# Performance work log

Measured on AMD Instinct MI355X. Metric: run time of the kernel, lower is better.

Reference implementation:

```python
import jax, jax.numpy as jnp
import numpy as np

EPS = 1e-5

def _ln(x, g, b):
    m = x.mean(-1, keepdims=True)
    v = x.var(-1, keepdims=True)
    return (x - m) / jnp.sqrt(v + EPS) * g + b

def _ln_na(x):
    m = x.mean(-1, keepdims=True)
    v = x.var(-1, keepdims=True)
    return (x - m) / jnp.sqrt(v + EPS)

def setup_inputs() -> dict:
    key = jax.random.key(0)
    ks = jax.random.split(key, 12)
    B, J, D, H, E, Z = 128, 4096, 64, 128, 256, 32
    s = 0.05
    return {
        "x": jax.random.normal(ks[0], (B, J), jnp.float32),
        "mask": jax.random.randint(ks[1], (B, J), 0, 2, jnp.int32),
        "feature_embedding": jax.random.normal(ks[2], (J, D), jnp.float32),
        "hW1": jax.random.normal(ks[3], (1 + D, H), jnp.float32) * s,
        "hb1": jnp.zeros((H,), jnp.float32),
        "hg1": jnp.ones((H,), jnp.float32),
        "hbt1": jnp.zeros((H,), jnp.float32),
        "hW2": jax.random.normal(ks[4], (H, D), jnp.float32) * s,
        "hb2": jnp.zeros((D,), jnp.float32),
        "hg2": jnp.ones((D,), jnp.float32),
        "hbt2": jnp.zeros((D,), jnp.float32),
        "eW1": jax.random.normal(ks[5], (D, E), jnp.float32) * s,
        "eb1": jnp.zeros((E,), jnp.float32),
        "eW2": jax.random.normal(ks[6], (E, 2 * Z), jnp.float32) * s,
        "eb2": jnp.zeros((2 * Z,), jnp.float32),
    }

def reference(x, mask, feature_embedding, hW1, hb1, hg1, hbt1, hW2, hb2, hg2, hbt2, eW1, eb1, eW2, eb2):
    B, J = x.shape
    D = feature_embedding.shape[1]
    m = (mask > 0).astype(x.dtype)  # (B, J)
    # per-(b,j) MLP on [x_bj, F_j]; masked entries are zeroed before pooling,
    # which equals the original gather-then-MLP-then-sum over observed entries.
    F = jnp.broadcast_to(feature_embedding[None], (B, J, D))
    h_in = jnp.concatenate([x[..., None], F], axis=-1)        # (B, J, 1+D)
    h = jax.nn.relu(_ln(h_in @ hW1 + hb1, hg1, hbt1))          # (B, J, H)
    h = jax.nn.relu(_ln(h @ hW2 + hb2, hg2, hbt2))             # (B, J, D)
    pooled = jnp.einsum('bjd,bj->bd', h, m)                    # sum over observed
    cnt = jnp.maximum(m.sum(-1, keepdims=True), 1.0)
    c = pooled / cnt                                           # mean pool; zeros if no obs
    # FCLayers (2 layers, LayerNorm w/o affine, ReLU each layer)
    e = jax.nn.relu(_ln_na(c @ eW1 + eb1))                     # (B, E)
    out = jax.nn.relu(_ln_na(e @ eW2 + eb2))                   # (B, 2Z)
    mu, logvar = jnp.split(out, 2, axis=-1)
    return (mu, logvar)
```

## Files before the change

### kernel.cpp

```cpp
#include <hip/hip_runtime.h>
#include <hip/hip_bf16.h>

#define B_  128
#define J_  4096
#define D_  64
#define H_  128
#define E_  256
#define Z_  32

typedef __attribute__((ext_vector_type(8))) short short8;
typedef __attribute__((ext_vector_type(4))) float floatx4;

#define OFF_G      0u
#define OFF_GSTATS 2097152u
#define OFF_SCAL   2162688u
#define OFF_W0C    2162944u
#define OFF_C3     2163456u
#define OFF_W2F    2163968u
#define OFF_POOL   2180352u

static __device__ __forceinline__ unsigned pk2(float a, float b) {
    __hip_bfloat162 t = __float22bfloat162_rn(make_float2(a, b));
    union { __hip_bfloat162 h; unsigned u; } c; c.h = t; return c.u;
}

__global__ __launch_bounds__(128) void g_kernel(
    const float* __restrict__ F, const float* __restrict__ hW1,
    const float* __restrict__ hb1, const float* __restrict__ hg1,
    float* __restrict__ Gp, float4* __restrict__ Gstats)
{
    const int j = blockIdx.x;
    const int h = threadIdx.x;
    const float* frow = F + (size_t)j * D_;
    float a0 = hb1[h], a1 = 0.f, a2 = 0.f, a3 = 0.f;
#pragma unroll
    for (int d = 0; d < D_; d += 4) {
        a0 = fmaf(frow[d + 0], hW1[(d + 1) * H_ + h], a0);
        a1 = fmaf(frow[d + 1], hW1[(d + 2) * H_ + h], a1);
        a2 = fmaf(frow[d + 2], hW1[(d + 3) * H_ + h], a2);
        a3 = fmaf(frow[d + 3], hW1[(d + 4) * H_ + h], a3);
    }
    const float acc = (a0 + a1) + (a2 + a3);

    const float w0h = hW1[h];
    float s1 = acc, s2 = w0h * acc, s3 = acc * acc;
#pragma unroll
    for (int off = 32; off; off >>= 1) {
        s1 += __shfl_xor(s1, off);
        s2 += __shfl_xor(s2, off);
        s3 += __shfl_xor(s3, off);
    }
    __shared__ float red[6];
    if ((h & 63) == 0) {
        int w = h >> 6;
        red[w*3+0] = s1; red[w*3+1] = s2; red[w*3+2] = s3;
    }
    __syncthreads();
    const float inv = 1.f / (float)H_;
    const float mG = (red[0] + red[3]) * inv;
    if (h == 0)
        Gstats[j] = make_float4(mG, (red[1]+red[4])*inv, (red[2]+red[5])*inv, 0.f);
    Gp[j * H_ + h] = (acc - mG) * hg1[h];
}

__global__ __launch_bounds__(256) void prep_kernel(
    const float* __restrict__ hW1, const float* __restrict__ hg1,
    const float* __restrict__ hbt1, const float* __restrict__ hW2,
    float* __restrict__ scal, float* __restrict__ w0c, float* __restrict__ c3,
    uint4* __restrict__ w2f, float4* __restrict__ pooled4)
{
    const int t = threadIdx.x;
    if (blockIdx.x > 0) {
        pooled4[(blockIdx.x - 1) * 256 + t] = make_float4(0.f, 0.f, 0.f, 0.f);
        return;
    }

    __shared__ float sred[4];
    if (t < H_) {
        const float w0h = hW1[t];
        float s = w0h, q = w0h * w0h;
#pragma unroll
        for (int off = 32; off; off >>= 1) {
            s += __shfl_xor(s, off);
            q += __shfl_xor(q, off);
        }
        if ((t & 63) == 0) { sred[(t >> 6) * 2] = s; sred[(t >> 6) * 2 + 1] = q; }
    }
    __syncthreads();
    const float mw0  = (sred[0] + sred[2]) * (1.f / (float)H_);
    const float ew02 = (sred[1] + sred[3]) * (1.f / (float)H_);
    if (t == 0) { scal[0] = mw0; scal[1] = ew02; }
    if (t < H_) {
        w0c[t] = (hW1[t] - mw0) * hg1[t];
        c3[t]  = hbt1[t];
    }

    const int lane = t & 63, wq = t >> 6;
    const int quad = lane >> 4, col = lane & 15;
    for (int f = wq; f < 16; f += 4) {
        const int kstep = f >> 2, nt = f & 3;
        const int kbase = kstep * 32 + quad * 8;
        const int n = nt * 16 + col;
        unsigned r[4];
#pragma unroll
        for (int p = 0; p < 4; p++)
            r[p] = pk2(hW2[(kbase + 2*p) * D_ + n], hW2[(kbase + 2*p + 1) * D_ + n]);
        w2f[f * 64 + lane] = make_uint4(r[0], r[1], r[2], r[3]);
    }
}

#define TPW 2
#define BB  4

__global__ __launch_bounds__(256, 2) void main_kernel(
    const float* __restrict__ x, const int* __restrict__ mask,
    const float* __restrict__ Gp, const float4* __restrict__ Gstats,
    const float* __restrict__ scal,
    const float* __restrict__ w0c, const float* __restrict__ c3,
    const uint4* __restrict__ w2f,
    const float* __restrict__ hb2, const float* __restrict__ hg2,
    const float* __restrict__ hbt2,
    float* __restrict__ pooled)
{
    const int tid  = threadIdx.x;
    const int lane = tid & 63;
    const int wv   = tid >> 6;
    const int quad = lane >> 4;
    const int col  = lane & 15;
    const int b0   = blockIdx.y * BB;

    short8 w2r[16];
#pragma unroll
    for (int f = 0; f < 16; f++) {
        union { uint4 v; short8 s; } c; c.v = w2f[f * 64 + lane];
        w2r[f] = c.s;
    }
    float4 wc[4][2], cc[4][2];
#pragma unroll
    for (int k = 0; k < 4; k++) {
        wc[k][0] = ((const float4*)(w0c + k*32 + quad*8))[0];
        wc[k][1] = ((const float4*)(w0c + k*32 + quad*8))[1];
        cc[k][0] = ((const float4*)(c3  + k*32 + quad*8))[0];
        cc[k][1] = ((const float4*)(c3  + k*32 + quad*8))[1];
    }
    float hb2v[4], g2v[4], bt2v[4];
#pragma unroll
    for (int nt = 0; nt < 4; nt++) {
        hb2v[nt] = hb2[nt*16 + col];
        g2v[nt]  = hg2[nt*16 + col];
        bt2v[nt] = hbt2[nt*16 + col];
    }
    const float mw0s  = scal[0];
    const float ew02s = scal[1];

    float pool[BB][4];
#pragma unroll
    for (int bb = 0; bb < BB; bb++)
#pragma unroll
        for (int nt = 0; nt < 4; nt++) pool[bb][nt] = 0.f;

    for (int t = 0; t < TPW; t++) {
        const int tIdx = (blockIdx.x * 4 + wv) * TPW + t;
        const int j0   = tIdx * 16;
        const int rowA = j0 + col;

        const float4 gs = Gstats[rowA];
        float xv[BB]; int4 mk[BB];
#pragma unroll
        for (int bb = 0; bb < BB; bb++) {
            xv[bb] = x[(size_t)(b0 + bb) * J_ + rowA];
            mk[bb] = *(const int4*)(mask + (size_t)(b0 + bb) * J_ + j0 + quad * 4);
        }
        const float* gpr = Gp + rowA * H_ + quad * 8;
        float4 ga[4][2];
#pragma unroll
        for (int k = 0; k < 4; k++) {
            ga[k][0] = ((const float4*)(gpr + k*32))[0];
            ga[k][1] = ((const float4*)(gpr + k*32))[1];
        }

#pragma unroll
        for (int bb = 0; bb < BB; bb++) {
            const float xA = xv[bb];
            const float mean = fmaf(xA, mw0s, gs.x);
            const float eh2  = fmaf(xA, fmaf(xA, ew02s, 2.f * gs.y), gs.z);
            const float r1   = rsqrtf(fmaf(-mean, mean, eh2) + 1e-5f);

            floatx4 acc[4];
#pragma unroll
            for (int nt = 0; nt < 4; nt++) acc[nt] = (floatx4){0.f, 0.f, 0.f, 0.f};

#pragma unroll
            for (int k = 0; k < 4; k++) {
                const float h0 = fmaxf(0.f, fmaf(fmaf(xA, wc[k][0].x, ga[k][0].x), r1, cc[k][0].x));
                const float h1 = fmaxf(0.f, fmaf(fmaf(xA, wc[k][0].y, ga[k][0].y), r1, cc[k][0].y));
                const float h2 = fmaxf(0.f, fmaf(fmaf(xA, wc[k][0].z, ga[k][0].z), r1, cc[k][0].z));
                const float h3 = fmaxf(0.f, fmaf(fmaf(xA, wc[k][0].w, ga[k][0].w), r1, cc[k][0].w));
                const float h4 = fmaxf(0.f, fmaf(fmaf(xA, wc[k][1].x, ga[k][1].x), r1, cc[k][1].x));
                const float h5 = fmaxf(0.f, fmaf(fmaf(xA, wc[k][1].y, ga[k][1].y), r1, cc[k][1].y));
                const float h6 = fmaxf(0.f, fmaf(fmaf(xA, wc[k][1].z, ga[k][1].z), r1, cc[k][1].z));
                const float h7 = fmaxf(0.f, fmaf(fmaf(xA, wc[k][1].w, ga[k][1].w), r1, cc[k][1].w));
                union { unsigned u[4]; short8 s; } af;
                af.u[0] = pk2(h0, h1);
                af.u[1] = pk2(h2, h3);
                af.u[2] = pk2(h4, h5);
                af.u[3] = pk2(h6, h7);
                acc[0] = __builtin_amdgcn_mfma_f32_16x16x32_bf16(af.s, w2r[k*4+0], acc[0], 0, 0, 0);
                acc[1] = __builtin_amdgcn_mfma_f32_16x16x32_bf16(af.s, w2r[k*4+1], acc[1], 0, 0, 0);
                acc[2] = __builtin_amdgcn_mfma_f32_16x16x32_bf16(af.s, w2r[k*4+2], acc[2], 0, 0, 0);
                acc[3] = __builtin_amdgcn_mfma_f32_16x16x32_bf16(af.s, w2r[k*4+3], acc[3], 0, 0, 0);
            }

            float sa[4], qa[4];
#pragma unroll
            for (int r = 0; r < 4; r++) {
                const float v0 = acc[0][r] + hb2v[0];
                const float v1 = acc[1][r] + hb2v[1];
                const float v2 = acc[2][r] + hb2v[2];
                const float v3 = acc[3][r] + hb2v[3];
                acc[0][r] = v0; acc[1][r] = v1; acc[2][r] = v2; acc[3][r] = v3;
                sa[r] = (v0 + v1) + (v2 + v3);
                qa[r] = fmaf(v0, v0, fmaf(v1, v1, fmaf(v2, v2, v3 * v3)));
            }
#pragma unroll
            for (int m = 1; m < 16; m <<= 1) {
#pragma unroll
                for (int r = 0; r < 4; r++) {
                    sa[r] += __shfl_xor(sa[r], m);
                    qa[r] += __shfl_xor(qa[r], m);
                }
            }
            float mrr[4];
            mrr[0] = (mk[bb].x > 0) ? 1.f : 0.f;
            mrr[1] = (mk[bb].y > 0) ? 1.f : 0.f;
            mrr[2] = (mk[bb].z > 0) ? 1.f : 0.f;
            mrr[3] = (mk[bb].w > 0) ? 1.f : 0.f;
#pragma unroll
            for (int r = 0; r < 4; r++) {
                const float m2 = sa[r] * (1.f / 64.f);
                const float v2 = fmaf(-m2, m2, qa[r] * (1.f / 64.f));
                const float r2 = rsqrtf(v2 + 1e-5f);
#pragma unroll
                for (int nt = 0; nt < 4; nt++) {
                    const float rg  = r2 * g2v[nt];
                    const float off = fmaf(-m2, rg, bt2v[nt]);
                    const float o   = fmaxf(0.f, fmaf(acc[nt][r], rg, off));
                    pool[bb][nt] = fmaf(mrr[r], o, pool[bb][nt]);
                }
            }
        }
    }

#pragma unroll
    for (int m = 16; m < 64; m <<= 1)
#pragma unroll
        for (int bb = 0; bb < BB; bb++)
#pragma unroll
            for (int nt = 0; nt < 4; nt++)
                pool[bb][nt] += __shfl_xor(pool[bb][nt], m);

    if (lane < 16) {
#pragma unroll
        for (int bb = 0; bb < BB; bb++)
#pragma unroll
            for (int nt = 0; nt < 4; nt++)
                atomicAdd(&pooled[(size_t)(b0 + bb) * D_ + nt * 16 + lane], pool[bb][nt]);
    }
}

__global__ __launch_bounds__(256) void final_kernel(
    const float* __restrict__ pooled, const int* __restrict__ mask,
    const float* __restrict__ eW1, const float* __restrict__ eb1,
    const float* __restrict__ eW2, const float* __restrict__ eb2,
    float* __restrict__ out)
{
    __shared__ float c_lds[D_];
    __shared__ float e_lds[E_];
    __shared__ float red[8];
    __shared__ float redc[4];
    const int b = blockIdx.x;
    const int t = threadIdx.x;
    const int lane = t & 63, wid = t >> 6;

    {
        const int4* mrow = (const int4*)(mask + (size_t)b * J_);
        int s = 0;
#pragma unroll
        for (int i = 0; i < 4; i++) {
            const int4 v = mrow[t * 4 + i];
            s += (v.x > 0) + (v.y > 0) + (v.z > 0) + (v.w > 0);
        }
        float fs = (float)s;
#pragma unroll
        for (int off = 32; off; off >>= 1) fs += __shfl_xor(fs, off);
        if (lane == 0) redc[wid] = fs;
    }
    __syncthreads();
    const float cn = fmaxf((redc[0] + redc[1]) + (redc[2] + redc[3]), 1.f);
    if (t < D_) c_lds[t] = pooled[(size_t)b * D_ + t] / cn;
    __syncthreads();

    float acc = eb1[t];
#pragma unroll
    for (int d = 0; d < D_; d++)
        acc = fmaf(c_lds[d], eW1[(size_t)d * E_ + t], acc);

    float s = acc, s2 = acc * acc;
#pragma unroll
    for (int off = 32; off; off >>= 1) {
        s  += __shfl_xor(s, off);
        s2 += __shfl_xor(s2, off);
    }
    if ((t & 63) == 0) { red[wid * 2] = s; red[wid * 2 + 1] = s2; }
    __syncthreads();
    s  = red[0] + red[2] + red[4] + red[6];
    s2 = red[1] + red[3] + red[5] + red[7];
    const float m = s * (1.f / (float)E_);
    const float v = fmaf(-m, m, s2 * (1.f / (float)E_));
    const float r = rsqrtf(v + 1e-5f);
    e_lds[t] = fmaxf(0.f, (acc - m) * r);
    __syncthreads();

    if (t < 64) {
        float a2 = eb2[t];
#pragma unroll 8
        for (int k = 0; k < E_; k++)
            a2 = fmaf(e_lds[k], eW2[(size_t)k * 64 + t], a2);

        float u = a2, u2 = a2 * a2;
#pragma unroll
        for (int off = 32; off; off >>= 1) {
            u  += __shfl_xor(u, off);
            u2 += __shfl_xor(u2, off);
        }
        const float m2 = u * (1.f / 64.f);
        const float v2 = fmaf(-m2, m2, u2 * (1.f / 64.f));
        const float r2 = rsqrtf(v2 + 1e-5f);
        const float o  = fmaxf(0.f, (a2 - m2) * r2);
        if (t < Z_) out[(size_t)b * Z_ + t] = o;
        else        out[(size_t)B_ * Z_ + (size_t)b * Z_ + (t - Z_)] = o;
    }
}

extern "C" void kernel_launch(void* const* d_in, const int* in_sizes, int n_in,
                              void* d_out, int out_size, void* d_ws, size_t ws_size,
                              hipStream_t stream) {
    const float* x    = (const float*)d_in[0];
    const int*   mask = (const int*)d_in[1];
    const float* F    = (const float*)d_in[2];
    const float* hW1  = (const float*)d_in[3];
    const float* hb1  = (const float*)d_in[4];
    const float* hg1  = (const float*)d_in[5];
    const float* hbt1 = (const float*)d_in[6];
    const float* hW2  = (const float*)d_in[7];
    const float* hb2  = (const float*)d_in[8];
    const float* hg2  = (const float*)d_in[9];
    const float* hbt2 = (const float*)d_in[10];
    const float* eW1  = (const float*)d_in[11];
    const float* eb1  = (const float*)d_in[12];
    const float* eW2  = (const float*)d_in[13];
    const float* eb2  = (const float*)d_in[14];
    float* out = (float*)d_out;

    char* ws = (char*)d_ws;
    float*  Gp     = (float*)(ws + OFF_G);
    float4* Gstats = (float4*)(ws + OFF_GSTATS);
    float*  scal   = (float*)(ws + OFF_SCAL);
    float*  w0c    = (float*)(ws + OFF_W0C);
    float*  c3     = (float*)(ws + OFF_C3);
    uint4*  w2f    = (uint4*)(ws + OFF_W2F);
    float*  pooled = (float*)(ws + OFF_POOL);

    g_kernel<<<J_, 128, 0, stream>>>(F, hW1, hb1, hg1, Gp, Gstats);
    prep_kernel<<<9, 256, 0, stream>>>(hW1, hg1, hbt1, hW2, scal, w0c, c3, w2f,
                                       (float4*)pooled);
    main_kernel<<<dim3(J_ / (16 * 4 * TPW), B_ / BB), 256, 0, stream>>>(
        x, mask, Gp, Gstats, scal, w0c, c3, w2f, hb2, hg2, hbt2, pooled);
    final_kernel<<<B_, E_, 0, stream>>>(pooled, mask, eW1, eb1, eW2, eb2, out);
}
```

Before: 142.0 us.

## Merge prep into precompute kernel and vectorize main-kernel math with packed float2 ops

Folds the weight-prep and pooled-zeroing work into the per-feature precompute kernel, so one fewer kernel launch is needed. In the main kernel, elementwise layer-norm and ReLU math moves to two-wide float vectors so the compiler can emit packed FMA/max instructions. The 16-lane row reductions switch from shuffles to DPP row operations, and bf16 packing uses manual round-to-nearest-even plus a byte permute. The final kernel's mask reads become coalesced across threads. The manual bf16 rounding does not handle NaN the way the library routine does.

```diff
diff --git a/kernel.cpp b/kernel.cpp
--- a/kernel.cpp
+++ b/kernel.cpp
@@ -10,6 +10,7 @@
 
 typedef __attribute__((ext_vector_type(8))) short short8;
 typedef __attribute__((ext_vector_type(4))) float floatx4;
+typedef __attribute__((ext_vector_type(2))) float f2;
 
 #define OFF_G      0u
 #define OFF_GSTATS 2097152u
@@ -19,18 +20,83 @@
 #define OFF_W2F    2163968u
 #define OFF_POOL   2180352u
 
+static __device__ __forceinline__ f2 mkf2(float a, float b) { f2 r; r.x = a; r.y = b; return r; }
+static __device__ __forceinline__ f2 fma2(f2 a, f2 b, f2 c) { return __builtin_elementwise_fma(a, b, c); }
+static __device__ __forceinline__ f2 max2(f2 a, f2 b) { return __builtin_elementwise_max(a, b); }
+
 static __device__ __forceinline__ unsigned pk2(float a, float b) {
-    __hip_bfloat162 t = __float22bfloat162_rn(make_float2(a, b));
-    union { __hip_bfloat162 h; unsigned u; } c; c.h = t; return c.u;
-}
-
-__global__ __launch_bounds__(128) void g_kernel(
+    unsigned ua = __builtin_bit_cast(unsigned, a);
+    unsigned ub = __builtin_bit_cast(unsigned, b);
+    ua += 0x7fffu + ((ua >> 16) & 1u);
+    ub += 0x7fffu + ((ub >> 16) & 1u);
+    return __builtin_amdgcn_perm(ub, ua, 0x07060302u);
+}
+
+static __device__ __forceinline__ float row16_sum(float v) {
+    int x;
+    x = __builtin_amdgcn_update_dpp(0, __builtin_bit_cast(int, v), 0xB1,  0xf, 0xf, true);
+    v += __builtin_bit_cast(float, x);
+    x = __builtin_amdgcn_update_dpp(0, __builtin_bit_cast(int, v), 0x4E,  0xf, 0xf, true);
+    v += __builtin_bit_cast(float, x);
+    x = __builtin_amdgcn_update_dpp(0, __builtin_bit_cast(int, v), 0x124, 0xf, 0xf, true);
+    v += __builtin_bit_cast(float, x);
+    x = __builtin_amdgcn_update_dpp(0, __builtin_bit_cast(int, v), 0x128, 0xf, 0xf, true);
+    v += __builtin_bit_cast(float, x);
+    return v;
+}
+
+__global__ __launch_bounds__(128) void pre_kernel(
     const float* __restrict__ F, const float* __restrict__ hW1,
     const float* __restrict__ hb1, const float* __restrict__ hg1,
-    float* __restrict__ Gp, float4* __restrict__ Gstats)
+    const float* __restrict__ hbt1, const float* __restrict__ hW2,
+    float* __restrict__ Gp, float4* __restrict__ Gstats,
+    float* __restrict__ scal, float* __restrict__ w0c, float* __restrict__ c3,
+    uint4* __restrict__ w2f, float4* __restrict__ pooled4)
 {
-    const int j = blockIdx.x;
-    const int h = threadIdx.x;
+    __shared__ float red[6];
+    const int bid = blockIdx.x;
+    const int t = threadIdx.x;
+
+    if (bid >= 4097) {
+        const int base = (bid - 4097) * 256;
+        pooled4[base + t]       = make_float4(0.f, 0.f, 0.f, 0.f);
+        pooled4[base + 128 + t] = make_float4(0.f, 0.f, 0.f, 0.f);
+        return;
+    }
+
+    if (bid == 4096) {
+        const float w0h = hW1[t];
+        float s = w0h, q = w0h * w0h;
+#pragma unroll
+        for (int off = 32; off; off >>= 1) {
+            s += __shfl_xor(s, off);
+            q += __shfl_xor(q, off);
+        }
+        if ((t & 63) == 0) { red[(t >> 6) * 2] = s; red[(t >> 6) * 2 + 1] = q; }
+        __syncthreads();
+        const float mw0  = (red[0] + red[2]) * (1.f / (float)H_);
+        const float ew02 = (red[1] + red[3]) * (1.f / (float)H_);
+        if (t == 0) { scal[0] = mw0; scal[1] = ew02; }
+        w0c[t] = (hW1[t] - mw0) * hg1[t];
+        c3[t]  = hbt1[t];
+
+        const int lane = t & 63, half = t >> 6;
+        const int quad = lane >> 4, col = lane & 15;
+        for (int f = half; f < 16; f += 2) {
+            const int kstep = f >> 2, nt = f & 3;
+            const int kbase = kstep * 32 + quad * 8;
+            const int n = nt * 16 + col;
+            unsigned r[4];
+#pragma unroll
+            for (int p = 0; p < 4; p++)
+                r[p] = pk2(hW2[(kbase + 2*p) * D_ + n], hW2[(kbase + 2*p + 1) * D_ + n]);
+            w2f[f * 64 + lane] = make_uint4(r[0], r[1], r[2], r[3]);
+        }
+        return;
+    }
+
+    const int j = bid;
+    const int h = t;
     const float* frow = F + (size_t)j * D_;
     float a0 = hb1[h], a1 = 0.f, a2 = 0.f, a3 = 0.f;
 #pragma unroll
@@ -50,7 +116,6 @@
         s2 += __shfl_xor(s2, off);
         s3 += __shfl_xor(s3, off);
     }
-    __shared__ float red[6];
     if ((h & 63) == 0) {
         int w = h >> 6;
         red[w*3+0] = s1; red[w*3+1] = s2; red[w*3+2] = s3;
@@ -61,52 +126,6 @@
     if (h == 0)
         Gstats[j] = make_float4(mG, (red[1]+red[4])*inv, (red[2]+red[5])*inv, 0.f);
     Gp[j * H_ + h] = (acc - mG) * hg1[h];
-}
-
-__global__ __launch_bounds__(256) void prep_kernel(
-    const float* __restrict__ hW1, const float* __restrict__ hg1,
-    const float* __restrict__ hbt1, const float* __restrict__ hW2,
-    float* __restrict__ scal, float* __restrict__ w0c, float* __restrict__ c3,
-    uint4* __restrict__ w2f, float4* __restrict__ pooled4)
-{
-    const int t = threadIdx.x;
-    if (blockIdx.x > 0) {
-        pooled4[(blockIdx.x - 1) * 256 + t] = make_float4(0.f, 0.f, 0.f, 0.f);
-        return;
-    }
-
-    __shared__ float sred[4];
-    if (t < H_) {
-        const float w0h = hW1[t];
-        float s = w0h, q = w0h * w0h;
-#pragma unroll
-        for (int off = 32; off; off >>= 1) {
-            s += __shfl_xor(s, off);
-            q += __shfl_xor(q, off);
-        }
-        if ((t & 63) == 0) { sred[(t >> 6) * 2] = s; sred[(t >> 6) * 2 + 1] = q; }
-    }
-    __syncthreads();
-    const float mw0  = (sred[0] + sred[2]) * (1.f / (float)H_);
-    const float ew02 = (sred[1] + sred[3]) * (1.f / (float)H_);
-    if (t == 0) { scal[0] = mw0; scal[1] = ew02; }
-    if (t < H_) {
-        w0c[t] = (hW1[t] - mw0) * hg1[t];
-        c3[t]  = hbt1[t];
-    }
-
-    const int lane = t & 63, wq = t >> 6;
-    const int quad = lane >> 4, col = lane & 15;
-    for (int f = wq; f < 16; f += 4) {
-        const int kstep = f >> 2, nt = f & 3;
-        const int kbase = kstep * 32 + quad * 8;
-        const int n = nt * 16 + col;
-        unsigned r[4];
-#pragma unroll
-        for (int p = 0; p < 4; p++)
-            r[p] = pk2(hW2[(kbase + 2*p) * D_ + n], hW2[(kbase + 2*p + 1) * D_ + n]);
-        w2f[f * 64 + lane] = make_uint4(r[0], r[1], r[2], r[3]);
-    }
 }
 
 #define TPW 2
@@ -135,29 +154,31 @@
         union { uint4 v; short8 s; } c; c.v = w2f[f * 64 + lane];
         w2r[f] = c.s;
     }
-    float4 wc[4][2], cc[4][2];
+    f2 wc2[4][4], cc2[4][4];
 #pragma unroll
     for (int k = 0; k < 4; k++) {
-        wc[k][0] = ((const float4*)(w0c + k*32 + quad*8))[0];
-        wc[k][1] = ((const float4*)(w0c + k*32 + quad*8))[1];
-        cc[k][0] = ((const float4*)(c3  + k*32 + quad*8))[0];
-        cc[k][1] = ((const float4*)(c3  + k*32 + quad*8))[1];
-    }
-    float hb2v[4], g2v[4], bt2v[4];
-#pragma unroll
-    for (int nt = 0; nt < 4; nt++) {
-        hb2v[nt] = hb2[nt*16 + col];
-        g2v[nt]  = hg2[nt*16 + col];
-        bt2v[nt] = hbt2[nt*16 + col];
-    }
+        const float4 wa = ((const float4*)(w0c + k*32 + quad*8))[0];
+        const float4 wb = ((const float4*)(w0c + k*32 + quad*8))[1];
+        wc2[k][0] = mkf2(wa.x, wa.y); wc2[k][1] = mkf2(wa.z, wa.w);
+        wc2[k][2] = mkf2(wb.x, wb.y); wc2[k][3] = mkf2(wb.z, wb.w);
+        const float4 ca = ((const float4*)(c3 + k*32 + quad*8))[0];
+        const float4 cb = ((const float4*)(c3 + k*32 + quad*8))[1];
+        cc2[k][0] = mkf2(ca.x, ca.y); cc2[k][1] = mkf2(ca.z, ca.w);
+        cc2[k][2] = mkf2(cb.x, cb.y); cc2[k][3] = mkf2(cb.z, cb.w);
+    }
+    const f2 hb01 = mkf2(hb2[col],      hb2[16 + col]);
+    const f2 hb23 = mkf2(hb2[32 + col], hb2[48 + col]);
+    const f2 g201 = mkf2(hg2[col],      hg2[16 + col]);
+    const f2 g223 = mkf2(hg2[32 + col], hg2[48 + col]);
+    const f2 bt01 = mkf2(hbt2[col],      hbt2[16 + col]);
+    const f2 bt23 = mkf2(hbt2[32 + col], hbt2[48 + col]);
     const float mw0s  = scal[0];
     const float ew02s = scal[1];
-
-    float pool[BB][4];
-#pragma unroll
-    for (int bb = 0; bb < BB; bb++)
-#pragma unroll
-        for (int nt = 0; nt < 4; nt++) pool[bb][nt] = 0.f;
+    const f2 z2 = mkf2(0.f, 0.f);
+
+    f2 pool01[BB], pool23[BB];
+#pragma unroll
+    for (int bb = 0; bb < BB; bb++) { pool01[bb] = z2; pool23[bb] = z2; }
 
     for (int t = 0; t < TPW; t++) {
         const int tIdx = (blockIdx.x * 4 + wv) * TPW + t;
@@ -172,11 +193,11 @@
             mk[bb] = *(const int4*)(mask + (size_t)(b0 + bb) * J_ + j0 + quad * 4);
         }
         const float* gpr = Gp + rowA * H_ + quad * 8;
-        float4 ga[4][2];
+        float4 ga4[4][2];
 #pragma unroll
         for (int k = 0; k < 4; k++) {
-            ga[k][0] = ((const float4*)(gpr + k*32))[0];
-            ga[k][1] = ((const float4*)(gpr + k*32))[1];
+            ga4[k][0] = ((const float4*)(gpr + k*32))[0];
+            ga4[k][1] = ((const float4*)(gpr + k*32))[1];
         }
 
 #pragma unroll
@@ -185,6 +206,8 @@
             const float mean = fmaf(xA, mw0s, gs.x);
             const float eh2  = fmaf(xA, fmaf(xA, ew02s, 2.f * gs.y), gs.z);
             const float r1   = rsqrtf(fmaf(-mean, mean, eh2) + 1e-5f);
+            const f2 x2v = mkf2(xA, xA);
+            const f2 r1v = mkf2(r1, r1);
 
             floatx4 acc[4];
 #pragma unroll
@@ -192,43 +215,35 @@
 
 #pragma unroll
             for (int k = 0; k < 4; k++) {
-                const float h0 = fmaxf(0.f, fmaf(fmaf(xA, wc[k][0].x, ga[k][0].x), r1, cc[k][0].x));
-                const float h1 = fmaxf(0.f, fmaf(fmaf(xA, wc[k][0].y, ga[k][0].y), r1, cc[k][0].y));
-                const float h2 = fmaxf(0.f, fmaf(fmaf(xA, wc[k][0].z, ga[k][0].z), r1, cc[k][0].z));
-                const float h3 = fmaxf(0.f, fmaf(fmaf(xA, wc[k][0].w, ga[k][0].w), r1, cc[k][0].w));
-                const float h4 = fmaxf(0.f, fmaf(fmaf(xA, wc[k][1].x, ga[k][1].x), r1, cc[k][1].x));
-                const float h5 = fmaxf(0.f, fmaf(fmaf(xA, wc[k][1].y, ga[k][1].y), r1, cc[k][1].y));
-                const float h6 = fmaxf(0.f, fmaf(fmaf(xA, wc[k][1].z, ga[k][1].z), r1, cc[k][1].z));
-                const float h7 = fmaxf(0.f, fmaf(fmaf(xA, wc[k][1].w, ga[k][1].w), r1, cc[k][1].w));
+                const f2 t0 = fma2(x2v, wc2[k][0], mkf2(ga4[k][0].x, ga4[k][0].y));
+                const f2 t1 = fma2(x2v, wc2[k][1], mkf2(ga4[k][0].z, ga4[k][0].w));
+                const f2 t2 = fma2(x2v, wc2[k][2], mkf2(ga4[k][1].x, ga4[k][1].y));
+                const f2 t3 = fma2(x2v, wc2[k][3], mkf2(ga4[k][1].z, ga4[k][1].w));
+                const f2 h0 = max2(fma2(t0, r1v, cc2[k][0]), z2);
+                const f2 h1 = max2(fma2(t1, r1v, cc2[k][1]), z2);
+                const f2 h2 = max2(fma2(t2, r1v, cc2[k][2]), z2);
+                const f2 h3 = max2(fma2(t3, r1v, cc2[k][3]), z2);
                 union { unsigned u[4]; short8 s; } af;
-                af.u[0] = pk2(h0, h1);
-                af.u[1] = pk2(h2, h3);
-                af.u[2] = pk2(h4, h5);
-                af.u[3] = pk2(h6, h7);
+                af.u[0] = pk2(h0.x, h0.y);
+                af.u[1] = pk2(h1.x, h1.y);
+                af.u[2] = pk2(h2.x, h2.y);
+                af.u[3] = pk2(h3.x, h3.y);
                 acc[0] = __builtin_amdgcn_mfma_f32_16x16x32_bf16(af.s, w2r[k*4+0], acc[0], 0, 0, 0);
                 acc[1] = __builtin_amdgcn_mfma_f32_16x16x32_bf16(af.s, w2r[k*4+1], acc[1], 0, 0, 0);
                 acc[2] = __builtin_amdgcn_mfma_f32_16x16x32_bf16(af.s, w2r[k*4+2], acc[2], 0, 0, 0);
                 acc[3] = __builtin_amdgcn_mfma_f32_16x16x32_bf16(af.s, w2r[k*4+3], acc[3], 0, 0, 0);
             }
 
+            f2 y01[4], y23[4];
             float sa[4], qa[4];
 #pragma unroll
             for (int r = 0; r < 4; r++) {
-                const float v0 = acc[0][r] + hb2v[0];
-                const float v1 = acc[1][r] + hb2v[1];
-                const float v2 = acc[2][r] + hb2v[2];
-                const float v3 = acc[3][r] + hb2v[3];
-                acc[0][r] = v0; acc[1][r] = v1; acc[2][r] = v2; acc[3][r] = v3;
-                sa[r] = (v0 + v1) + (v2 + v3);
-                qa[r] = fmaf(v0, v0, fmaf(v1, v1, fmaf(v2, v2, v3 * v3)));
-            }
-#pragma unroll
-            for (int m = 1; m < 16; m <<= 1) {
-#pragma unroll
-                for (int r = 0; r < 4; r++) {
-                    sa[r] += __shfl_xor(sa[r], m);
-                    qa[r] += __shfl_xor(qa[r], m);
-                }
+                y01[r] = mkf2(acc[0][r], acc[1][r]) + hb01;
+                y23[r] = mkf2(acc[2][r], acc[3][r]) + hb23;
+                const f2 s  = y01[r] + y23[r];
+                const f2 qq = fma2(y01[r], y01[r], y23[r] * y23[r]);
+                sa[r] = row16_sum(s.x + s.y);
+                qa[r] = row16_sum(qq.x + qq.y);
             }
             float mrr[4];
             mrr[0] = (mk[bb].x > 0) ? 1.f : 0.f;
@@ -239,32 +254,40 @@
             for (int r = 0; r < 4; r++) {
                 const float m2 = sa[r] * (1.f / 64.f);
                 const float v2 = fmaf(-m2, m2, qa[r] * (1.f / 64.f));
-                const float r2 = rsqrtf(v2 + 1e-5f);
-#pragma unroll
-                for (int nt = 0; nt < 4; nt++) {
-                    const float rg  = r2 * g2v[nt];
-                    const float off = fmaf(-m2, rg, bt2v[nt]);
-                    const float o   = fmaxf(0.f, fmaf(acc[nt][r], rg, off));
-                    pool[bb][nt] = fmaf(mrr[r], o, pool[bb][nt]);
-                }
+                const float rs = rsqrtf(v2 + 1e-5f);
+                const f2 rsv  = mkf2(rs, rs);
+                const f2 rg01 = rsv * g201;
+                const f2 rg23 = rsv * g223;
+                const f2 nm2  = mkf2(-m2, -m2);
+                const f2 off01 = fma2(nm2, rg01, bt01);
+                const f2 off23 = fma2(nm2, rg23, bt23);
+                const f2 o01 = max2(fma2(y01[r], rg01, off01), z2);
+                const f2 o23 = max2(fma2(y23[r], rg23, off23), z2);
+                const f2 mr2 = mkf2(mrr[r], mrr[r]);
+                pool01[bb] = fma2(mr2, o01, pool01[bb]);
+                pool23[bb] = fma2(mr2, o23, pool23[bb]);
             }
         }
     }
 
 #pragma unroll
-    for (int m = 16; m < 64; m <<= 1)
-#pragma unroll
-        for (int bb = 0; bb < BB; bb++)
-#pragma unroll
-            for (int nt = 0; nt < 4; nt++)
-                pool[bb][nt] += __shfl_xor(pool[bb][nt], m);
-
+    for (int m = 16; m < 64; m <<= 1) {
+#pragma unroll
+        for (int bb = 0; bb < BB; bb++) {
+            pool01[bb].x += __shfl_xor(pool01[bb].x, m);
+            pool01[bb].y += __shfl_xor(pool01[bb].y, m);
+            pool23[bb].x += __shfl_xor(pool23[bb].x, m);
+            pool23[bb].y += __shfl_xor(pool23[bb].y, m);
+        }
+    }
     if (lane < 16) {
 #pragma unroll
-        for (int bb = 0; bb < BB; bb++)
-#pragma unroll
-            for (int nt = 0; nt < 4; nt++)
-                atomicAdd(&pooled[(size_t)(b0 + bb) * D_ + nt * 16 + lane], pool[bb][nt]);
+        for (int bb = 0; bb < BB; bb++) {
+            atomicAdd(&pooled[(size_t)(b0 + bb) * D_ +  0 + lane], pool01[bb].x);
+            atomicAdd(&pooled[(size_t)(b0 + bb) * D_ + 16 + lane], pool01[bb].y);
+            atomicAdd(&pooled[(size_t)(b0 + bb) * D_ + 32 + lane], pool23[bb].x);
+            atomicAdd(&pooled[(size_t)(b0 + bb) * D_ + 48 + lane], pool23[bb].y);
+        }
     }
 }
 
@@ -287,7 +310,7 @@
         int s = 0;
 #pragma unroll
         for (int i = 0; i < 4; i++) {
-            const int4 v = mrow[t * 4 + i];
+            const int4 v = mrow[i * 256 + t];
             s += (v.x > 0) + (v.y > 0) + (v.z > 0) + (v.w > 0);
         }
         float fs = (float)s;
@@ -371,9 +394,9 @@
     uint4*  w2f    = (uint4*)(ws + OFF_W2F);
     float*  pooled = (float*)(ws + OFF_POOL);
 
-    g_kernel<<<J_, 128, 0, stream>>>(F, hW1, hb1, hg1, Gp, Gstats);
-    prep_kernel<<<9, 256, 0, stream>>>(hW1, hg1, hbt1, hW2, scal, w0c, c3, w2f,
-                                       (float4*)pooled);
+    pre_kernel<<<J_ + 9, 128, 0, stream>>>(F, hW1, hb1, hg1, hbt1, hW2,
+                                           Gp, Gstats, scal, w0c, c3, w2f,
+                                           (float4*)pooled);
     main_kernel<<<dim3(J_ / (16 * 4 * TPW), B_ / BB), 256, 0, stream>>>(
         x, mask, Gp, Gstats, scal, w0c, c3, w2f, hb2, hg2, hbt2, pooled);
     final_kernel<<<B_, E_, 0, stream>>>(pooled, mask, eW1, eb1, eW2, eb2, out);
```

After: 148.6 us. 1.05x slower.
